# Optimization experiments

Measured on AMD Instinct MI355X. Metric: run time of the kernel, lower is better.

## Reference

```python
import jax, jax.numpy as jnp
import numpy as np

TOP_K = 2

def setup_inputs() -> dict:
    key = jax.random.key(0)
    k1, k2, k3, k4, k5 = jax.random.split(key, 5)
    B, S, H, E, F = 2, 1024, 1024, 8, 2816
    scale = 0.02
    return {
        "hidden_states": jax.random.normal(k1, (B, S, H), dtype=jnp.float32),
        "gate_w": jax.random.normal(k2, (E, H), dtype=jnp.float32) * scale,
        "w1": jax.random.normal(k3, (E, H, F), dtype=jnp.float32) * scale,
        "w3": jax.random.normal(k4, (E, H, F), dtype=jnp.float32) * scale,
        "w2": jax.random.normal(k5, (E, F, H), dtype=jnp.float32) * scale,
    }

def reference(hidden_states, gate_w, w1, w3, w2):
    B, S, H = hidden_states.shape
    E = gate_w.shape[0]
    x = hidden_states.reshape(-1, H)                      # [T, H]
    T = x.shape[0]
    # Router: logits -> fp32 softmax -> top-k -> renormalize
    router_logits = jnp.einsum('th,eh->te', x, gate_w)    # [T, E]
    probs = jax.nn.softmax(router_logits.astype(jnp.float32), axis=-1)
    top_w, top_i = jax.lax.top_k(probs, TOP_K)            # [T, k]
    top_w = top_w / jnp.sum(top_w, axis=-1, keepdims=True)
    # Scatter normalized top-k weights into dense combine matrix [T, E]
    combine = jnp.zeros((T, E), dtype=probs.dtype)
    combine = combine.at[jnp.arange(T)[:, None], top_i].set(top_w)
    combine = combine.astype(x.dtype)
    # Experts: SwiGLU MLP per expert, weighted combine (dense formulation
    # of gather -> grouped GEMM -> scatter; non-selected experts get weight 0)
    g = jnp.einsum('th,ehf->tef', x, w1)                  # gate proj
    u = jnp.einsum('th,ehf->tef', x, w3)                  # up proj
    act = jax.nn.silu(g) * u                              # [T, E, F]
    act = act * combine[:, :, None]                       # apply routing weight
    out = jnp.einsum('tef,efh->th', act, w2)              # down proj + combine
    final_hidden_states = out.reshape(B, S, H)
    return final_hidden_states, router_logits
```

## Files before the change

### kernel.cpp

```cpp
#include <hip/hip_runtime.h>

typedef unsigned short u16;
typedef unsigned int u32;
typedef __attribute__((ext_vector_type(8))) short bf16x8;
typedef __attribute__((ext_vector_type(4))) float f32x4;

#define T_TOK 2048
#define H_DIM 1024
#define E_NUM 8
#define F_DIM 2816
#define BM 128
#define BN1 128
#define BN2 64
#define BK1 32
#define BK2 64
#define SPLITF 2
#define FS (F_DIM / SPLITF)
#define LDK1 40
#define LDK2 72

__device__ __forceinline__ u16 f2bf(float f) {
    u32 b = __float_as_uint(f);
    u32 lsb = (b >> 16) & 1u;
    b += 0x7fffu + lsb;
    return (u16)(b >> 16);
}

__global__ __launch_bounds__(64) void router_kernel(
    const float* __restrict__ x, const float* __restrict__ gw,
    float* __restrict__ logits_out, int* __restrict__ cnt,
    int* __restrict__ tok_list, float* __restrict__ wt_list)
{
    int t = blockIdx.x;
    int lane = threadIdx.x;
    const float* xr = x + (size_t)t * H_DIM;

    float acc[E_NUM];
#pragma unroll
    for (int e = 0; e < E_NUM; e++) acc[e] = 0.f;

    for (int j = 0; j < H_DIM / 64; j++) {
        int idx = j * 64 + lane;
        float xv = xr[idx];
#pragma unroll
        for (int e = 0; e < E_NUM; e++)
            acc[e] += xv * gw[e * H_DIM + idx];
    }
#pragma unroll
    for (int e = 0; e < E_NUM; e++) {
        float v = acc[e];
#pragma unroll
        for (int o = 32; o > 0; o >>= 1) v += __shfl_xor(v, o, 64);
        acc[e] = v;
    }
    if (lane == 0) {
#pragma unroll
        for (int e = 0; e < E_NUM; e++) logits_out[t * E_NUM + e] = acc[e];
        float m = acc[0];
#pragma unroll
        for (int e = 1; e < E_NUM; e++) m = fmaxf(m, acc[e]);
        float p[E_NUM], s = 0.f;
#pragma unroll
        for (int e = 0; e < E_NUM; e++) { p[e] = expf(acc[e] - m); s += p[e]; }
        float inv = 1.f / s;
#pragma unroll
        for (int e = 0; e < E_NUM; e++) p[e] *= inv;
        int i0 = 0;
#pragma unroll
        for (int e = 1; e < E_NUM; e++) if (p[e] > p[i0]) i0 = e;
        int i1 = (i0 == 0) ? 1 : 0;
#pragma unroll
        for (int e = 0; e < E_NUM; e++) if (e != i0 && p[e] > p[i1]) i1 = e;
        float w0 = p[i0], w1 = p[i1];
        float rs = 1.f / (w0 + w1);
        w0 *= rs; w1 *= rs;
        int s0 = atomicAdd(&cnt[i0], 1);
        tok_list[i0 * T_TOK + s0] = t; wt_list[i0 * T_TOK + s0] = w0;
        int s1 = atomicAdd(&cnt[i1], 1);
        tok_list[i1 * T_TOK + s1] = t; wt_list[i1 * T_TOK + s1] = w1;
    }
}

__global__ void offsets_kernel(const int* __restrict__ cnt, int* __restrict__ off)
{
    if (threadIdx.x == 0 && blockIdx.x == 0) {
        int s = 0;
        for (int e = 0; e < E_NUM; e++) {
            off[e] = s;
            s += ((cnt[e] + BM - 1) / BM) * BM;
        }
    }
}

__global__ __launch_bounds__(256, 2) void gemm1_kernel(
    const float* __restrict__ x, const float* __restrict__ w1,
    const float* __restrict__ w3, const int* __restrict__ cnt,
    const int* __restrict__ off, const int* __restrict__ tok_list,
    const float* __restrict__ wt_list, u16* __restrict__ act)
{
    int e = blockIdx.z;
    int m0 = blockIdx.y * BM;
    int n0 = blockIdx.x * BN1;
    if (m0 >= cnt[e]) return;

    __shared__ __align__(16) u16 As[BM][LDK1];
    __shared__ __align__(16) u16 B1[BN1][LDK1];
    __shared__ __align__(16) u16 B3[BN1][LDK1];
    __shared__ int tok_s[BM];
    __shared__ float wt_s[BM];

    int tid = threadIdx.x;
    if (tid < BM) {
        int tok = tok_list[e * T_TOK + m0 + tid];
        tok_s[tid] = tok;
        wt_s[tid] = (tok >= 0) ? wt_list[e * T_TOK + m0 + tid] : 0.f;
    }
    __syncthreads();

    int wid = tid >> 6, lane = tid & 63, q = lane >> 4, l15 = lane & 15;
    int wr = (wid >> 1) * 64, wc = (wid & 1) * 64;

    const f32x4 zero = {0.f, 0.f, 0.f, 0.f};
    f32x4 accg[4][4], accu[4][4];
#pragma unroll
    for (int i = 0; i < 4; i++)
#pragma unroll
        for (int j = 0; j < 4; j++) { accg[i][j] = zero; accu[i][j] = zero; }

    const int arow = tid >> 1, ah = (tid & 1) * 16;
    const int tokA = tok_s[arow];
    const float* xbase = x + (tokA >= 0 ? (size_t)tokA * H_DIM + ah : 0);
    const int bf = tid & 127, bk0 = (tid >> 7) * 16;
    const size_t wb = (size_t)e * H_DIM * F_DIM + n0 + bf;

    float a16[16], b1v[16], b3v[16];
#pragma unroll
    for (int j = 0; j < 16; j++) a16[j] = 0.f;

    {
        if (tokA >= 0) {
            const float4* xr = (const float4*)(xbase + 0);
            *(float4*)&a16[0] = xr[0]; *(float4*)&a16[4] = xr[1];
            *(float4*)&a16[8] = xr[2]; *(float4*)&a16[12] = xr[3];
        }
        const size_t base = wb + (size_t)bk0 * F_DIM;
#pragma unroll
        for (int j = 0; j < 16; j++) {
            b1v[j] = w1[base + (size_t)j * F_DIM];
            b3v[j] = w3[base + (size_t)j * F_DIM];
        }
    }

    const int NIT = H_DIM / BK1;
    for (int it = 0; it < NIT; ++it) {
        {
            union { uint4 v[2]; u16 u[16]; } pu;
#pragma unroll
            for (int j = 0; j < 16; j++) pu.u[j] = f2bf(a16[j]);
            *(uint4*)&As[arow][ah]     = pu.v[0];
            *(uint4*)&As[arow][ah + 8] = pu.v[1];
#pragma unroll
            for (int j = 0; j < 16; j++) pu.u[j] = f2bf(b1v[j]);
            *(uint4*)&B1[bf][bk0]     = pu.v[0];
            *(uint4*)&B1[bf][bk0 + 8] = pu.v[1];
#pragma unroll
            for (int j = 0; j < 16; j++) pu.u[j] = f2bf(b3v[j]);
            *(uint4*)&B3[bf][bk0]     = pu.v[0];
            *(uint4*)&B3[bf][bk0 + 8] = pu.v[1];
        }
        __syncthreads();

        if (it + 1 < NIT) {
            const int k0n = (it + 1) * BK1;
            if (tokA >= 0) {
                const float4* xr = (const float4*)(xbase + k0n);
                *(float4*)&a16[0] = xr[0]; *(float4*)&a16[4] = xr[1];
                *(float4*)&a16[8] = xr[2]; *(float4*)&a16[12] = xr[3];
            }
            const size_t base = wb + (size_t)(k0n + bk0) * F_DIM;
#pragma unroll
            for (int j = 0; j < 16; j++) {
                b1v[j] = w1[base + (size_t)j * F_DIM];
                b3v[j] = w3[base + (size_t)j * F_DIM];
            }
        }

        bf16x8 a[4], f1[4], f3[4];
#pragma unroll
        for (int tm = 0; tm < 4; tm++)
            a[tm] = *(const bf16x8*)&As[wr + tm * 16 + l15][q * 8];
#pragma unroll
        for (int tn = 0; tn < 4; tn++) {
            f1[tn] = *(const bf16x8*)&B1[wc + tn * 16 + l15][q * 8];
            f3[tn] = *(const bf16x8*)&B3[wc + tn * 16 + l15][q * 8];
        }
#pragma unroll
        for (int tm = 0; tm < 4; tm++)
#pragma unroll
            for (int tn = 0; tn < 4; tn++) {
                accg[tm][tn] = __builtin_amdgcn_mfma_f32_16x16x32_bf16(a[tm], f1[tn], accg[tm][tn], 0, 0, 0);
                accu[tm][tn] = __builtin_amdgcn_mfma_f32_16x16x32_bf16(a[tm], f3[tn], accu[tm][tn], 0, 0, 0);
            }
        __syncthreads();
    }

    const int pos0 = off[e] + m0;
#pragma unroll
    for (int tm = 0; tm < 4; tm++) {
        const int row = wr + tm * 16 + q * 4;
#pragma unroll
        for (int r = 0; r < 4; r++) {
            const float wt = wt_s[row + r];
            u16* aptr = act + (size_t)(pos0 + row + r) * F_DIM + n0 + wc + l15;
#pragma unroll
            for (int tn = 0; tn < 4; tn++) {
                float g = accg[tm][tn][r];
                float u = accu[tm][tn][r];
                float sg = g / (1.f + expf(-g));
                aptr[tn * 16] = f2bf(sg * u * wt);
            }
        }
    }
}

__global__ __launch_bounds__(256, 3) void gemm2_kernel(
    const u16* __restrict__ act, const float* __restrict__ w2,
    const int* __restrict__ cnt, const int* __restrict__ off,
    const int* __restrict__ tok_list, float* __restrict__ out)
{
    int e  = blockIdx.z / SPLITF;
    int ks = blockIdx.z % SPLITF;
    int m0 = blockIdx.y * BM;
    int n0 = blockIdx.x * BN2;
    if (m0 >= cnt[e]) return;

    __shared__ __align__(16) u16 As[BM][LDK2];
    __shared__ __align__(16) u16 Bt[BN2][LDK2];
    __shared__ int tok_s[BM];

    int tid = threadIdx.x;
    if (tid < BM) tok_s[tid] = tok_list[e * T_TOK + m0 + tid];
    __syncthreads();

    int wid = tid >> 6, lane = tid & 63, q = lane >> 4, l15 = lane & 15;
    int wr = (wid >> 1) * 64, wc = (wid & 1) * 32;

    const f32x4 zero = {0.f, 0.f, 0.f, 0.f};
    f32x4 acc[4][2];
#pragma unroll
    for (int i = 0; i < 4; i++)
#pragma unroll
        for (int j = 0; j < 2; j++) acc[i][j] = zero;

    const int arow = tid >> 1, ah = (tid & 1) * 32;
    const u16* abase = act + (size_t)(off[e] + m0 + arow) * F_DIM + ah + (size_t)ks * FS;
    const int bh = tid & 63, bk0 = (tid >> 6) * 16;
    const float* wbase = w2 + (size_t)e * F_DIM * H_DIM + n0 + bh + (size_t)(ks * FS + bk0) * H_DIM;

    uint4 av[4];
    float bv[16];

    {
#pragma unroll
        for (int j = 0; j < 4; j++) av[j] = *(const uint4*)(abase + j * 8);
#pragma unroll
        for (int j = 0; j < 16; j++) bv[j] = wbase[(size_t)j * H_DIM];
    }

    const int NIT = FS / BK2;
    for (int it = 0; it < NIT; ++it) {
#pragma unroll
        for (int j = 0; j < 4; j++) *(uint4*)&As[arow][ah + j * 8] = av[j];
        {
            union { uint4 v[2]; u16 u[16]; } pu;
#pragma unroll
            for (int j = 0; j < 16; j++) pu.u[j] = f2bf(bv[j]);
            *(uint4*)&Bt[bh][bk0]     = pu.v[0];
            *(uint4*)&Bt[bh][bk0 + 8] = pu.v[1];
        }
        __syncthreads();

        if (it + 1 < NIT) {
            const int k0n = (it + 1) * BK2;
#pragma unroll
            for (int j = 0; j < 4; j++) av[j] = *(const uint4*)(abase + k0n + j * 8);
            const float* wnext = wbase + (size_t)k0n * H_DIM;
#pragma unroll
            for (int j = 0; j < 16; j++) bv[j] = wnext[(size_t)j * H_DIM];
        }

#pragma unroll
        for (int kk = 0; kk < 2; ++kk) {
            bf16x8 a[4], b[2];
#pragma unroll
            for (int tm = 0; tm < 4; tm++)
                a[tm] = *(const bf16x8*)&As[wr + tm * 16 + l15][kk * 32 + q * 8];
#pragma unroll
            for (int tn = 0; tn < 2; tn++)
                b[tn] = *(const bf16x8*)&Bt[wc + tn * 16 + l15][kk * 32 + q * 8];
#pragma unroll
            for (int tm = 0; tm < 4; tm++)
#pragma unroll
                for (int tn = 0; tn < 2; tn++)
                    acc[tm][tn] = __builtin_amdgcn_mfma_f32_16x16x32_bf16(a[tm], b[tn], acc[tm][tn], 0, 0, 0);
        }
        __syncthreads();
    }

#pragma unroll
    for (int tm = 0; tm < 4; tm++) {
        const int row = wr + tm * 16 + q * 4;
#pragma unroll
        for (int r = 0; r < 4; r++) {
            const int tok = tok_s[row + r];
            if (tok >= 0) {
                float* optr = out + (size_t)tok * H_DIM + n0 + wc + l15;
#pragma unroll
                for (int tn = 0; tn < 2; tn++)
                    atomicAdd(&optr[tn * 16], acc[tm][tn][r]);
            }
        }
    }
}

extern "C" void kernel_launch(void* const* d_in, const int* in_sizes, int n_in,
                              void* d_out, int out_size, void* d_ws, size_t ws_size,
                              hipStream_t stream) {
    const float* x  = (const float*)d_in[0];
    const float* gw = (const float*)d_in[1];
    const float* w1 = (const float*)d_in[2];
    const float* w3 = (const float*)d_in[3];
    const float* w2 = (const float*)d_in[4];
    float* out = (float*)d_out;

    char* ws = (char*)d_ws;
    int*   cnt      = (int*)(ws);
    int*   off      = (int*)(ws + 64);
    int*   tok_list = (int*)(ws + 128);
    float* wt_list  = (float*)(ws + 128 + 65536);
    u16*   act      = (u16*)(ws + 128 + 131072);

    hipMemsetAsync(cnt, 0, 64, stream);
    hipMemsetAsync(tok_list, 0xFF, 65536, stream);
    hipMemsetAsync(out, 0, (size_t)T_TOK * H_DIM * sizeof(float), stream);

    float* logits_out = out + (size_t)T_TOK * H_DIM;
    router_kernel<<<T_TOK, 64, 0, stream>>>(x, gw, logits_out, cnt, tok_list, wt_list);
    offsets_kernel<<<1, 64, 0, stream>>>(cnt, off);
    gemm1_kernel<<<dim3(F_DIM / BN1, T_TOK / BM, E_NUM), 256, 0, stream>>>(
        x, w1, w3, cnt, off, tok_list, wt_list, act);
    gemm2_kernel<<<dim3(H_DIM / BN2, T_TOK / BM, E_NUM * SPLITF), 256, 0, stream>>>(
        act, w2, cnt, off, tok_list, out);
}
```

Measured before the change: 590.6 us.

## Replace atomic scatter in down-proj with per-row buffers and a gather combine kernel

The down-projection GEMM now writes its partial results as plain stores into a per-split row buffer instead of issuing float atomicAdds into the output. A new combine kernel gathers each token's two expert rows across the splits, using an inverse map built in the offsets kernel. The grids of both GEMMs are also reordered so that blocks for the same expert and the same N tile sit next to each other in blockIdx.x, which may help weight reuse in cache. In exchange the code needs a much larger workspace, does an extra full read and write pass over the row buffers, and falls back to the old atomic path when the workspace is too small.

```diff
diff --git a/kernel.cpp b/kernel.cpp
--- a/kernel.cpp
+++ b/kernel.cpp
@@ -14,10 +14,9 @@
 #define BN2 64
 #define BK1 32
 #define BK2 64
-#define SPLITF 2
-#define FS (F_DIM / SPLITF)
 #define LDK1 40
 #define LDK2 72
+#define ROWS_MAX 5120
 
 __device__ __forceinline__ u16 f2bf(float f) {
     u32 b = __float_as_uint(f);
@@ -81,13 +80,28 @@
     }
 }
 
-__global__ void offsets_kernel(const int* __restrict__ cnt, int* __restrict__ off)
+__global__ __launch_bounds__(256) void offsets_kernel(
+    const int* __restrict__ cnt, int* __restrict__ off,
+    const int* __restrict__ tok_list, int* __restrict__ inv)
 {
-    if (threadIdx.x == 0 && blockIdx.x == 0) {
+    __shared__ int soff[E_NUM];
+    __shared__ int tc[T_TOK];
+    int tid = threadIdx.x;
+    if (tid == 0) {
         int s = 0;
         for (int e = 0; e < E_NUM; e++) {
-            off[e] = s;
+            soff[e] = s; off[e] = s;
             s += ((cnt[e] + BM - 1) / BM) * BM;
+        }
+    }
+    for (int i = tid; i < T_TOK; i += 256) tc[i] = 0;
+    __syncthreads();
+    for (int e = 0; e < E_NUM; e++) {
+        int c = cnt[e];
+        for (int s = tid; s < c; s += 256) {
+            int t = tok_list[e * T_TOK + s];
+            int sl = atomicAdd(&tc[t], 1);
+            inv[t * 2 + sl] = soff[e] + s;
         }
     }
 }
@@ -98,9 +112,11 @@
     const int* __restrict__ off, const int* __restrict__ tok_list,
     const float* __restrict__ wt_list, u16* __restrict__ act)
 {
-    int e = blockIdx.z;
+    int pair = blockIdx.x;
+    int n_i  = pair % 22;
+    int e    = pair / 22;
     int m0 = blockIdx.y * BM;
-    int n0 = blockIdx.x * BN1;
+    int n0 = n_i * BN1;
     if (m0 >= cnt[e]) return;
 
     __shared__ __align__(16) u16 As[BM][LDK1];
@@ -223,15 +239,21 @@
     }
 }
 
+template<int NSPLIT, bool USE_ROWS>
 __global__ __launch_bounds__(256, 3) void gemm2_kernel(
     const u16* __restrict__ act, const float* __restrict__ w2,
     const int* __restrict__ cnt, const int* __restrict__ off,
-    const int* __restrict__ tok_list, float* __restrict__ out)
+    const int* __restrict__ tok_list, float* __restrict__ rows,
+    float* __restrict__ out)
 {
-    int e  = blockIdx.z / SPLITF;
-    int ks = blockIdx.z % SPLITF;
+    constexpr int FS = F_DIM / NSPLIT;
+    int pair = blockIdx.x;
+    int n_i  = pair & 15;
+    int rest = pair >> 4;
+    int e  = rest / NSPLIT;
+    int ks = rest % NSPLIT;
     int m0 = blockIdx.y * BM;
-    int n0 = blockIdx.x * BN2;
+    int n0 = n_i * BN2;
     if (m0 >= cnt[e]) return;
 
     __shared__ __align__(16) u16 As[BM][LDK2];
@@ -307,20 +329,55 @@
         __syncthreads();
     }
 
-#pragma unroll
-    for (int tm = 0; tm < 4; tm++) {
-        const int row = wr + tm * 16 + q * 4;
-#pragma unroll
-        for (int r = 0; r < 4; r++) {
-            const int tok = tok_s[row + r];
-            if (tok >= 0) {
-                float* optr = out + (size_t)tok * H_DIM + n0 + wc + l15;
+    if (USE_ROWS) {
+        float* rbase = rows + (size_t)ks * ((size_t)ROWS_MAX * H_DIM)
+                            + (size_t)(off[e] + m0) * H_DIM;
+#pragma unroll
+        for (int tm = 0; tm < 4; tm++) {
+            const int row = wr + tm * 16 + q * 4;
+#pragma unroll
+            for (int r = 0; r < 4; r++) {
+                float* rp = rbase + (size_t)(row + r) * H_DIM + n0 + wc + l15;
 #pragma unroll
                 for (int tn = 0; tn < 2; tn++)
-                    atomicAdd(&optr[tn * 16], acc[tm][tn][r]);
-            }
-        }
-    }
+                    rp[tn * 16] = acc[tm][tn][r];
+            }
+        }
+    } else {
+#pragma unroll
+        for (int tm = 0; tm < 4; tm++) {
+            const int row = wr + tm * 16 + q * 4;
+#pragma unroll
+            for (int r = 0; r < 4; r++) {
+                const int tok = tok_s[row + r];
+                if (tok >= 0) {
+                    float* optr = out + (size_t)tok * H_DIM + n0 + wc + l15;
+#pragma unroll
+                    for (int tn = 0; tn < 2; tn++)
+                        atomicAdd(&optr[tn * 16], acc[tm][tn][r]);
+                }
+            }
+        }
+    }
+}
+
+template<int NSPLIT>
+__global__ __launch_bounds__(256) void combine_kernel(
+    const float* __restrict__ rows, const int* __restrict__ inv,
+    float* __restrict__ out)
+{
+    int t = blockIdx.x;
+    int h = threadIdx.x * 4;
+    int p0 = inv[t * 2], p1 = inv[t * 2 + 1];
+    float4 s = {0.f, 0.f, 0.f, 0.f};
+#pragma unroll
+    for (int ks = 0; ks < NSPLIT; ks++) {
+        const float* r = rows + (size_t)ks * ((size_t)ROWS_MAX * H_DIM);
+        float4 a = *(const float4*)&r[(size_t)p0 * H_DIM + h];
+        float4 b = *(const float4*)&r[(size_t)p1 * H_DIM + h];
+        s.x += a.x + b.x; s.y += a.y + b.y; s.z += a.z + b.z; s.w += a.w + b.w;
+    }
+    *(float4*)&out[(size_t)t * H_DIM + h] = s;
 }
 
 extern "C" void kernel_launch(void* const* d_in, const int* in_sizes, int n_in,
@@ -338,7 +395,12 @@
     int*   off      = (int*)(ws + 64);
     int*   tok_list = (int*)(ws + 128);
     float* wt_list  = (float*)(ws + 128 + 65536);
-    u16*   act      = (u16*)(ws + 128 + 131072);
+    int*   inv      = (int*)(ws + 128 + 131072);
+    u16*   act      = (u16*)(ws + 147584);
+    const size_t act_bytes  = (size_t)ROWS_MAX * F_DIM * sizeof(u16);
+    float* rowsbuf  = (float*)(ws + 147584 + act_bytes);
+    const size_t rows_one   = (size_t)ROWS_MAX * H_DIM * sizeof(float);
+    const size_t base_need  = 147584 + act_bytes;
 
     hipMemsetAsync(cnt, 0, 64, stream);
     hipMemsetAsync(tok_list, 0xFF, 65536, stream);
@@ -346,9 +408,20 @@
 
     float* logits_out = out + (size_t)T_TOK * H_DIM;
     router_kernel<<<T_TOK, 64, 0, stream>>>(x, gw, logits_out, cnt, tok_list, wt_list);
-    offsets_kernel<<<1, 64, 0, stream>>>(cnt, off);
-    gemm1_kernel<<<dim3(F_DIM / BN1, T_TOK / BM, E_NUM), 256, 0, stream>>>(
+    offsets_kernel<<<1, 256, 0, stream>>>(cnt, off, tok_list, inv);
+    gemm1_kernel<<<dim3(22 * E_NUM, T_TOK / BM, 1), 256, 0, stream>>>(
         x, w1, w3, cnt, off, tok_list, wt_list, act);
-    gemm2_kernel<<<dim3(H_DIM / BN2, T_TOK / BM, E_NUM * SPLITF), 256, 0, stream>>>(
-        act, w2, cnt, off, tok_list, out);
-}
+
+    if (ws_size >= base_need + 2 * rows_one) {
+        gemm2_kernel<2, true><<<dim3(16 * E_NUM * 2, T_TOK / BM, 1), 256, 0, stream>>>(
+            act, w2, cnt, off, tok_list, rowsbuf, out);
+        combine_kernel<2><<<T_TOK, 256, 0, stream>>>(rowsbuf, inv, out);
+    } else if (ws_size >= base_need + rows_one) {
+        gemm2_kernel<1, true><<<dim3(16 * E_NUM, T_TOK / BM, 1), 256, 0, stream>>>(
+            act, w2, cnt, off, tok_list, rowsbuf, out);
+        combine_kernel<1><<<T_TOK, 256, 0, stream>>>(rowsbuf, inv, out);
+    } else {
+        gemm2_kernel<2, false><<<dim3(16 * E_NUM * 2, T_TOK / BM, 1), 256, 0, stream>>>(
+            act, w2, cnt, off, tok_list, nullptr, out);
+    }
+}
```

Measured after the change: 589.9 us. About the same (-0.1%).
